# Kernel optimization log

Measured on AMD Instinct MI355X. Metric: run time of the kernel, lower is better.

## Reference

```python
import jax, jax.numpy as jnp
import numpy as np

IDIM = 1024
ODIM = 1024
NHEADS = 16
B, S = 4, 1024


def setup_inputs() -> dict:
    key = jax.random.key(0)
    k1, k2, k3, k4, k5, k6 = jax.random.split(key, 6)
    m_feats = jax.random.normal(k1, (B, S, IDIM), dtype=jnp.float32)
    mask = jax.random.randint(k2, (B, S), 0, 2, dtype=jnp.int32)
    # torch Linear weights stored pre-transposed: y = x @ W + b
    W_c = jax.random.normal(k3, (IDIM, 2 * ODIM), dtype=jnp.float32) * 0.02
    b_c = jnp.zeros((2 * ODIM,), dtype=jnp.float32)
    W_v = jax.random.normal(k4, (IDIM, ODIM), dtype=jnp.float32) * 0.02
    b_v = jnp.zeros((ODIM,), dtype=jnp.float32)
    return {"m_feats": m_feats, "mask": mask, "W_c": W_c, "b_c": b_c, "W_v": W_v, "b_v": b_v}


def reference(m_feats, mask, W_c, b_c, W_v, b_v):
    # dp = 0.0 -> dropout is identity (eval-mode equivalence)
    Bn, Sn, _ = m_feats.shape
    odim = W_v.shape[1]
    dh = odim // NHEADS
    m_k = m_feats @ W_v + b_v            # v_lin  -> keys   [B,S,odim]
    m_trans = m_feats @ W_c + b_c        # c_lin  -> [B,S,2*odim]
    m_q = m_trans[..., :odim]            # queries
    m_v = m_trans[..., odim:]            # values
    mk = m_k.reshape(Bn, Sn, NHEADS, dh)
    mq = m_q.reshape(Bn, Sn, NHEADS, dh)
    mv = m_v.reshape(Bn, Sn, NHEADS, dh)
    # original: scores = K @ Q^T / sqrt(dh); softmax over the Q (last) axis
    scores = jnp.einsum('bihd,bjhd->bhij', mk, mq) / jnp.sqrt(jnp.float32(dh))
    maskf = mask.astype(jnp.float32)
    scores = jnp.where(maskf[:, None, None, :] == 0.0, jnp.float32(-1e9), scores)
    w = jax.nn.softmax(scores, axis=-1)               # [B,H,S,S]
    r = jnp.einsum('bhij,bjhd->bihd', w, mv).reshape(Bn, Sn, odim)
    updated_m = m_feats + r
    return updated_m, w
```

## Files before the change

### kernel.cpp

```cpp
#include <hip/hip_runtime.h>
#include <cstddef>

typedef short short8 __attribute__((ext_vector_type(8)));
typedef float f32x4 __attribute__((ext_vector_type(4)));

#define SS 1024
#define NH 16
#define DH 64
#define NB 4

static __device__ __forceinline__ unsigned short f2bf(float f) {
    union { float f; unsigned int i; } x; x.f = f;
    unsigned int r = x.i + 0x7FFFu + ((x.i >> 16) & 1u);
    return (unsigned short)(r >> 16);
}
static __device__ __forceinline__ float bf2f(unsigned short u) {
    union { unsigned int i; float f; } x; x.i = ((unsigned int)u) << 16;
    return x.f;
}

static __device__ __forceinline__ void g2l16(const void* g, void* l) {
    __builtin_amdgcn_global_load_lds(
        (const __attribute__((address_space(1))) unsigned int*)g,
        (__attribute__((address_space(3))) unsigned int*)l, 16, 0, 0);
}

__global__ __launch_bounds__(256) void prep(const float* __restrict__ mf,
                                            unsigned short* __restrict__ mfb,
                                            const float* __restrict__ Wv,
                                            const float* __restrict__ Wc,
                                            unsigned short* __restrict__ WT) {
    __shared__ float tile[32][33];
    int bx = blockIdx.x;
    int t = threadIdx.x;
    if (bx < 4096) {
        size_t i = ((size_t)bx * 256 + t) * 4;
        float4 v = *(const float4*)(mf + i);
        short4 o;
        o.x = (short)f2bf(v.x); o.y = (short)f2bf(v.y);
        o.z = (short)f2bf(v.z); o.w = (short)f2bf(v.w);
        *(short4*)(mfb + i) = o;
        return;
    }
    bx -= 4096;
    int n0 = (bx % 96) * 32, k0 = (bx / 96) * 32;
    int kr = t >> 3, nc = (t & 7) * 4;
    const float* src; int ld; int nn = n0 + nc;
    if (n0 < 1024) { src = Wv; ld = 1024; } else { src = Wc; ld = 2048; nn -= 1024; }
    float4 v = *(const float4*)(src + (size_t)(k0 + kr) * ld + nn);
    tile[kr][nc + 0] = v.x; tile[kr][nc + 1] = v.y;
    tile[kr][nc + 2] = v.z; tile[kr][nc + 3] = v.w;
    __syncthreads();
    int nr = t >> 3, kc = (t & 7) * 4;
    short4 o;
    o.x = (short)f2bf(tile[kc + 0][nr]); o.y = (short)f2bf(tile[kc + 1][nr]);
    o.z = (short)f2bf(tile[kc + 2][nr]); o.w = (short)f2bf(tile[kc + 3][nr]);
    *(short4*)(WT + (size_t)(n0 + nr) * 1024 + k0 + kc) = o;
}

__global__ __launch_bounds__(256) void gemm_kqv(const unsigned short* __restrict__ A,
                                                const unsigned short* __restrict__ BT,
                                                const float* __restrict__ bv,
                                                const float* __restrict__ bc,
                                                unsigned short* __restrict__ kq,
                                                unsigned short* __restrict__ mvT) {
    __shared__ __align__(16) unsigned short As[128 * 32];
    __shared__ __align__(16) unsigned short Bs[128 * 32];
    int lin = blockIdx.y * 24 + blockIdx.x;
    int xcd = lin & 7, idx = lin >> 3;
    int cx = xcd & 1, cy = xcd >> 1;
    int xi = idx % 12, yi = idx / 12;
    int n0 = (cx * 12 + xi) * 128;
    int m0 = (cy * 8 + yi) * 128;

    int tid = threadIdx.x, lane = tid & 63, wv = tid >> 6;
    int wm = wv >> 1, wn = wv & 1;
    int lq = lane & 15, quad = lane >> 4;

    f32x4 zero = {0.f, 0.f, 0.f, 0.f};
    f32x4 acc[4][4];
#pragma unroll
    for (int i = 0; i < 4; ++i)
#pragma unroll
        for (int j = 0; j < 4; ++j) acc[i][j] = zero;

    int r0 = tid >> 2, s0 = tid & 3;
    int c0 = s0 ^ ((r0 >> 1) & 3);
    int r1 = (tid + 256) >> 2, s1 = tid & 3;
    int c1 = s1 ^ ((r1 >> 1) & 3);

    const unsigned short* Abase0 = A + (size_t)(m0 + r0) * 1024 + c0 * 8;
    const unsigned short* Abase1 = A + (size_t)(m0 + r1) * 1024 + c1 * 8;
    const unsigned short* Bbase0 = BT + (size_t)(n0 + r0) * 1024 + c0 * 8;
    const unsigned short* Bbase1 = BT + (size_t)(n0 + r1) * 1024 + c1 * 8;

    for (int kt = 0; kt < 1024; kt += 32) {
        __syncthreads();
        g2l16(Abase0 + kt, As + tid * 8);
        g2l16(Abase1 + kt, As + (tid + 256) * 8);
        g2l16(Bbase0 + kt, Bs + tid * 8);
        g2l16(Bbase1 + kt, Bs + (tid + 256) * 8);
        __syncthreads();

        short8 af[4], bfr[4];
#pragma unroll
        for (int i = 0; i < 4; ++i) {
            int Ra = wm * 64 + i * 16 + lq;
            af[i] = *(const short8*)(As + Ra * 32 + (quad ^ ((Ra >> 1) & 3)) * 8);
            int Rb = wn * 64 + i * 16 + lq;
            bfr[i] = *(const short8*)(Bs + Rb * 32 + (quad ^ ((Rb >> 1) & 3)) * 8);
        }
#pragma unroll
        for (int mi = 0; mi < 4; ++mi)
#pragma unroll
            for (int ni = 0; ni < 4; ++ni)
                acc[mi][ni] = __builtin_amdgcn_mfma_f32_16x16x32_bf16(af[mi], bfr[ni], acc[mi][ni], 0, 0, 0);
    }

#pragma unroll
    for (int mi = 0; mi < 4; ++mi) {
#pragma unroll
        for (int ni = 0; ni < 4; ++ni) {
            int colg = n0 + wn * 64 + ni * 16 + lq;
            float bias = (colg < 1024) ? bv[colg] : bc[colg - 1024];
            if (colg < 2048) {
#pragma unroll
                for (int r = 0; r < 4; ++r) {
                    int rowg = m0 + wm * 64 + mi * 16 + quad * 4 + r;
                    kq[(size_t)rowg * 2048 + colg] = f2bf(acc[mi][ni][r] + bias);
                }
            } else {
                int c = colg - 2048;
                int hh = c >> 6, dd = c & 63;
#pragma unroll
                for (int r = 0; r < 4; ++r) {
                    int rowg = m0 + wm * 64 + mi * 16 + quad * 4 + r;
                    int bb = rowg >> 10, jj = rowg & 1023;
                    mvT[((size_t)(bb * NH + hh) * DH + dd) * 1024 + jj] =
                        f2bf(acc[mi][ni][r] + bias);
                }
            }
        }
    }
}

__global__ __launch_bounds__(256, 4) void attn_kernel(const unsigned short* __restrict__ kq,
                                                      const unsigned short* __restrict__ mvT,
                                                      const int* __restrict__ mask,
                                                      const float* __restrict__ m_feats,
                                                      float* __restrict__ out0,
                                                      float* __restrict__ out1) {
    __shared__ __align__(16) unsigned short mk_s[16 * 72];
    __shared__ __align__(16) unsigned short s_exp[16 * 1032];
    __shared__ float wsum[4][16];
    __shared__ float inv_s[16];

    int tid = threadIdx.x;
    int lane = tid & 63, wv = tid >> 6;
    int lq = lane & 15, quad = lane >> 4;

    int blk = ((int)blockIdx.x & 7) * 512 + ((int)blockIdx.x >> 3);
    int it = blk & 63;
    int bh = blk >> 6;
    int h = bh & (NH - 1), b = bh >> 4;
    int i0 = it * 16;

    const float SC = 0.18033688011112042f;
    const unsigned short* mqb = kq + (size_t)b * SS * 2048 + 1024 + h * 64 + quad * 8;
    const int* maskb = mask + (size_t)b * SS;

    short8 qb[2][4][2];
    int qm[2][4];
    float sums[4] = {0.f, 0.f, 0.f, 0.f};

#define QLOAD(p, s)                                                          \
    {                                                                        \
        int jb_ = (s) * 256 + wv * 64;                                       \
        _Pragma("unroll") for (int js = 0; js < 4; ++js) {                   \
            int jg_ = jb_ + js * 16 + lq;                                    \
            size_t ro_ = (size_t)jg_ * 2048;                                 \
            qb[p][js][0] = *(const short8*)(mqb + ro_);                      \
            qb[p][js][1] = *(const short8*)(mqb + ro_ + 32);                 \
            qm[p][js] = maskb[jg_];                                          \
        }                                                                    \
    }

#define QCOMP(p, s)                                                          \
    {                                                                        \
        int jb_ = (s) * 256 + wv * 64;                                       \
        _Pragma("unroll") for (int js = 0; js < 4; ++js) {                   \
            f32x4 acc = {0.f, 0.f, 0.f, 0.f};                                \
            acc = __builtin_amdgcn_mfma_f32_16x16x32_bf16(a0, qb[p][js][0], acc, 0, 0, 0); \
            acc = __builtin_amdgcn_mfma_f32_16x16x32_bf16(a1, qb[p][js][1], acc, 0, 0, 0); \
            int jc_ = jb_ + js * 16 + lq;                                    \
            _Pragma("unroll") for (int r = 0; r < 4; ++r) {                  \
                float e = qm[p][js] ? __builtin_amdgcn_exp2f(acc[r] * SC) : 0.f; \
                sums[r] += e;                                                \
                s_exp[(quad * 4 + r) * 1032 + jc_] = f2bf(e);                \
            }                                                                \
        }                                                                    \
    }

    QLOAD(0, 0);

    float mf4[4];
#pragma unroll
    for (int r = 0; r < 4; ++r) {
        size_t o = (size_t)(b * SS + i0 + quad * 4 + r) * 1024 + h * 64 + wv * 16 + lq;
        mf4[r] = m_feats[o];
    }

    if (tid < 128) {
        int row = tid >> 3, ch = tid & 7;
        int4 v = *(const int4*)(kq + (size_t)(b * SS + i0 + row) * 2048 + h * 64 + ch * 8);
        *(int4*)(mk_s + row * 72 + ch * 8) = v;
    }
    QLOAD(1, 1);
    __syncthreads();

    short8 a0 = *(const short8*)(mk_s + lq * 72 + 0 * 32 + quad * 8);
    short8 a1 = *(const short8*)(mk_s + lq * 72 + 1 * 32 + quad * 8);

    QCOMP(0, 0); QLOAD(0, 2);
    QCOMP(1, 1); QLOAD(1, 3);
    QCOMP(0, 2);
    QCOMP(1, 3);
#undef QLOAD
#undef QCOMP

#pragma unroll
    for (int r = 0; r < 4; ++r) {
        float s = sums[r];
        s += __shfl_xor(s, 1); s += __shfl_xor(s, 2);
        s += __shfl_xor(s, 4); s += __shfl_xor(s, 8);
        if (lq == 0) wsum[wv][quad * 4 + r] = s;
    }
    __syncthreads();
    if (tid < 16) {
        float s = wsum[0][tid] + wsum[1][tid] + wsum[2][tid] + wsum[3][tid];
        inv_s[tid] = 1.0f / s;
    }
    __syncthreads();

    f32x4 racc = {0.f, 0.f, 0.f, 0.f};
    const unsigned short* mvb = mvT + ((size_t)bh * DH + wv * 16 + lq) * 1024 + quad * 8;
    size_t wbase = ((size_t)bh * SS + i0) * SS;
    short8 vbuf[4][4];

#define VLOAD(p, ko)                                                         \
    {                                                                        \
        _Pragma("unroll") for (int k2 = 0; k2 < 4; ++k2)                     \
            vbuf[p][k2] = *(const short8*)(mvb + ((ko) * 4 + k2) * 32);      \
    }

#define VCOMP(p, ko)                                                         \
    {                                                                        \
        _Pragma("unroll") for (int k2 = 0; k2 < 4; ++k2) {                   \
            short8 ae = *(const short8*)(s_exp + lq * 1032 + ((ko) * 4 + k2) * 32 + quad * 8); \
            racc = __builtin_amdgcn_mfma_f32_16x16x32_bf16(ae, vbuf[p][k2], racc, 0, 0, 0); \
        }                                                                    \
    }

#define WOUT(r)                                                              \
    {                                                                        \
        float iv = inv_s[r];                                                 \
        short4 ev = *(const short4*)(s_exp + (r) * 1032 + tid * 4);          \
        f32x4 wo;                                                            \
        wo[0] = bf2f((unsigned short)ev.x) * iv;                             \
        wo[1] = bf2f((unsigned short)ev.y) * iv;                             \
        wo[2] = bf2f((unsigned short)ev.z) * iv;                             \
        wo[3] = bf2f((unsigned short)ev.w) * iv;                             \
        __builtin_nontemporal_store(wo, (f32x4*)(out1 + wbase + (size_t)(r) * SS + tid * 4)); \
    }

    VLOAD(0, 0); VLOAD(1, 1); VLOAD(2, 2); VLOAD(3, 3);
    VCOMP(0, 0); VLOAD(0, 4); WOUT(0);  WOUT(1);
    VCOMP(1, 1); VLOAD(1, 5); WOUT(2);  WOUT(3);
    VCOMP(2, 2); VLOAD(2, 6); WOUT(4);  WOUT(5);
    VCOMP(3, 3); VLOAD(3, 7); WOUT(6);  WOUT(7);
    VCOMP(0, 4); WOUT(8);  WOUT(9);
    VCOMP(1, 5); WOUT(10); WOUT(11);
    VCOMP(2, 6); WOUT(12); WOUT(13);
    VCOMP(3, 7); WOUT(14); WOUT(15);
#undef VLOAD
#undef VCOMP
#undef WOUT

#pragma unroll
    for (int r = 0; r < 4; ++r) {
        int row = quad * 4 + r;
        size_t o = (size_t)(b * SS + i0 + row) * 1024 + h * 64 + wv * 16 + lq;
        __builtin_nontemporal_store(mf4[r] + racc[r] * inv_s[row], out0 + o);
    }
}

extern "C" void kernel_launch(void* const* d_in, const int* in_sizes, int n_in,
                              void* d_out, int out_size, void* d_ws, size_t ws_size,
                              hipStream_t stream) {
    const float* m_feats = (const float*)d_in[0];
    const int*   mask    = (const int*)d_in[1];
    const float* W_c     = (const float*)d_in[2];
    const float* b_c     = (const float*)d_in[3];
    const float* W_v     = (const float*)d_in[4];
    const float* b_v     = (const float*)d_in[5];

    float* out0 = (float*)d_out;
    float* out1 = out0 + (size_t)NB * SS * 1024;

    unsigned short* mf_bf = (unsigned short*)d_ws;
    unsigned short* WT    = mf_bf + (size_t)4096 * 1024;
    unsigned short* kq    = WT + (size_t)3072 * 1024;
    unsigned short* mvT   = kq + (size_t)4096 * 2048;

    prep<<<dim3(7168), dim3(256), 0, stream>>>(m_feats, mf_bf, W_v, W_c, WT);
    gemm_kqv<<<dim3(24, 32), dim3(256), 0, stream>>>(mf_bf, WT, b_v, b_c, kq, mvT);
    attn_kernel<<<dim3(4096), dim3(256), 0, stream>>>(kq, mvT, mask, m_feats, out0, out1);
}
```

Before: 433.2 us.

## Double-buffer GEMM LDS tiles, widen prep conversion, overlap V loads with softmax sum

The GEMM now keeps two LDS buffers per operand and prefetches the next K tile with async global-to-LDS loads while MFMAs run on the current one. This cuts the syncs per iteration from two to one and hides load latency. The prep kernel converts 8 floats per thread instead of 4, halving its conversion block count. In the attention kernel, the softmax row-sum reduction is moved after the first V-fragment loads so those global loads overlap the shuffle and reduction. Double buffering doubles LDS use in the GEMM, which may reduce occupancy.

```diff
diff --git a/kernel.cpp b/kernel.cpp
--- a/kernel.cpp
+++ b/kernel.cpp
@@ -33,16 +33,19 @@
     __shared__ float tile[32][33];
     int bx = blockIdx.x;
     int t = threadIdx.x;
-    if (bx < 4096) {
-        size_t i = ((size_t)bx * 256 + t) * 4;
-        float4 v = *(const float4*)(mf + i);
-        short4 o;
-        o.x = (short)f2bf(v.x); o.y = (short)f2bf(v.y);
-        o.z = (short)f2bf(v.z); o.w = (short)f2bf(v.w);
-        *(short4*)(mfb + i) = o;
+    if (bx < 2048) {
+        size_t i = ((size_t)bx * 256 + t) * 8;
+        float4 v0 = *(const float4*)(mf + i);
+        float4 v1 = *(const float4*)(mf + i + 4);
+        short8 o;
+        o[0] = (short)f2bf(v0.x); o[1] = (short)f2bf(v0.y);
+        o[2] = (short)f2bf(v0.z); o[3] = (short)f2bf(v0.w);
+        o[4] = (short)f2bf(v1.x); o[5] = (short)f2bf(v1.y);
+        o[6] = (short)f2bf(v1.z); o[7] = (short)f2bf(v1.w);
+        *(short8*)(mfb + i) = o;
         return;
     }
-    bx -= 4096;
+    bx -= 2048;
     int n0 = (bx % 96) * 32, k0 = (bx / 96) * 32;
     int kr = t >> 3, nc = (t & 7) * 4;
     const float* src; int ld; int nn = n0 + nc;
@@ -64,8 +67,8 @@
                                                 const float* __restrict__ bc,
                                                 unsigned short* __restrict__ kq,
                                                 unsigned short* __restrict__ mvT) {
-    __shared__ __align__(16) unsigned short As[128 * 32];
-    __shared__ __align__(16) unsigned short Bs[128 * 32];
+    __shared__ __align__(16) unsigned short As[2][128 * 32];
+    __shared__ __align__(16) unsigned short Bs[2][128 * 32];
     int lin = blockIdx.y * 24 + blockIdx.x;
     int xcd = lin & 7, idx = lin >> 3;
     int cx = xcd & 1, cy = xcd >> 1;
@@ -94,27 +97,38 @@
     const unsigned short* Bbase0 = BT + (size_t)(n0 + r0) * 1024 + c0 * 8;
     const unsigned short* Bbase1 = BT + (size_t)(n0 + r1) * 1024 + c1 * 8;
 
-    for (int kt = 0; kt < 1024; kt += 32) {
-        __syncthreads();
-        g2l16(Abase0 + kt, As + tid * 8);
-        g2l16(Abase1 + kt, As + (tid + 256) * 8);
-        g2l16(Bbase0 + kt, Bs + tid * 8);
-        g2l16(Bbase1 + kt, Bs + (tid + 256) * 8);
-        __syncthreads();
+    g2l16(Abase0, As[0] + tid * 8);
+    g2l16(Abase1, As[0] + (tid + 256) * 8);
+    g2l16(Bbase0, Bs[0] + tid * 8);
+    g2l16(Bbase1, Bs[0] + (tid + 256) * 8);
+    __syncthreads();
+
+#pragma unroll 2
+    for (int t32 = 0; t32 < 32; ++t32) {
+        int cur = t32 & 1;
+        if (t32 < 31) {
+            int nkt = (t32 + 1) * 32;
+            g2l16(Abase0 + nkt, As[cur ^ 1] + tid * 8);
+            g2l16(Abase1 + nkt, As[cur ^ 1] + (tid + 256) * 8);
+            g2l16(Bbase0 + nkt, Bs[cur ^ 1] + tid * 8);
+            g2l16(Bbase1 + nkt, Bs[cur ^ 1] + (tid + 256) * 8);
+        }
 
         short8 af[4], bfr[4];
 #pragma unroll
         for (int i = 0; i < 4; ++i) {
             int Ra = wm * 64 + i * 16 + lq;
-            af[i] = *(const short8*)(As + Ra * 32 + (quad ^ ((Ra >> 1) & 3)) * 8);
+            af[i] = *(const short8*)(As[cur] + Ra * 32 + (quad ^ ((Ra >> 1) & 3)) * 8);
             int Rb = wn * 64 + i * 16 + lq;
-            bfr[i] = *(const short8*)(Bs + Rb * 32 + (quad ^ ((Rb >> 1) & 3)) * 8);
+            bfr[i] = *(const short8*)(Bs[cur] + Rb * 32 + (quad ^ ((Rb >> 1) & 3)) * 8);
         }
 #pragma unroll
         for (int mi = 0; mi < 4; ++mi)
 #pragma unroll
             for (int ni = 0; ni < 4; ++ni)
                 acc[mi][ni] = __builtin_amdgcn_mfma_f32_16x16x32_bf16(af[mi], bfr[ni], acc[mi][ni], 0, 0, 0);
+
+        __syncthreads();
     }
 
 #pragma unroll
@@ -228,20 +242,6 @@
 #undef QLOAD
 #undef QCOMP
 
-#pragma unroll
-    for (int r = 0; r < 4; ++r) {
-        float s = sums[r];
-        s += __shfl_xor(s, 1); s += __shfl_xor(s, 2);
-        s += __shfl_xor(s, 4); s += __shfl_xor(s, 8);
-        if (lq == 0) wsum[wv][quad * 4 + r] = s;
-    }
-    __syncthreads();
-    if (tid < 16) {
-        float s = wsum[0][tid] + wsum[1][tid] + wsum[2][tid] + wsum[3][tid];
-        inv_s[tid] = 1.0f / s;
-    }
-    __syncthreads();
-
     f32x4 racc = {0.f, 0.f, 0.f, 0.f};
     const unsigned short* mvb = mvT + ((size_t)bh * DH + wv * 16 + lq) * 1024 + quad * 8;
     size_t wbase = ((size_t)bh * SS + i0) * SS;
@@ -273,7 +273,23 @@
         __builtin_nontemporal_store(wo, (f32x4*)(out1 + wbase + (size_t)(r) * SS + tid * 4)); \
     }
 
-    VLOAD(0, 0); VLOAD(1, 1); VLOAD(2, 2); VLOAD(3, 3);
+    VLOAD(0, 0); VLOAD(1, 1);
+
+#pragma unroll
+    for (int r = 0; r < 4; ++r) {
+        float s = sums[r];
+        s += __shfl_xor(s, 1); s += __shfl_xor(s, 2);
+        s += __shfl_xor(s, 4); s += __shfl_xor(s, 8);
+        if (lq == 0) wsum[wv][quad * 4 + r] = s;
+    }
+    __syncthreads();
+    if (tid < 16) {
+        float s = wsum[0][tid] + wsum[1][tid] + wsum[2][tid] + wsum[3][tid];
+        inv_s[tid] = 1.0f / s;
+    }
+    VLOAD(2, 2); VLOAD(3, 3);
+    __syncthreads();
+
     VCOMP(0, 0); VLOAD(0, 4); WOUT(0);  WOUT(1);
     VCOMP(1, 1); VLOAD(1, 5); WOUT(2);  WOUT(3);
     VCOMP(2, 2); VLOAD(2, 6); WOUT(4);  WOUT(5);
@@ -312,7 +328,7 @@
     unsigned short* kq    = WT + (size_t)3072 * 1024;
     unsigned short* mvT   = kq + (size_t)4096 * 2048;
 
-    prep<<<dim3(7168), dim3(256), 0, stream>>>(m_feats, mf_bf, W_v, W_c, WT);
+    prep<<<dim3(5120), dim3(256), 0, stream>>>(m_feats, mf_bf, W_v, W_c, WT);
     gemm_kqv<<<dim3(24, 32), dim3(256), 0, stream>>>(mf_bf, WT, b_v, b_c, kq, mvT);
     attn_kernel<<<dim3(4096), dim3(256), 0, stream>>>(kq, mvT, mask, m_feats, out0, out1);
 }
```

Result: faster. 421.3 us (-2.8%).
